# Optimization experiments

Hardware: AMD Instinct MI355X
Metric: run time of the kernel (lower is better)

The kernel has to match this reference:

```python
import jax, jax.numpy as jnp
import numpy as np

HID = 128  # hardcoded in the original module (hyperparameters['hidden_sizes'])
BETA1, BETA2, ADAM_EPS = 0.9, 0.999, 1e-8  # torch.optim.Adam defaults


def _xavier(k, shape):
    lim = np.sqrt(6.0 / (shape[0] + shape[1]))
    return jax.random.uniform(k, shape, jnp.float32, -lim, lim)


def setup_inputs() -> dict:
    key = jax.random.key(0)
    k0, k1, k2 = jax.random.split(key, 3)
    input_size, output_size = 65536, 4096
    return {
        "x": jax.random.uniform(k0, (input_size,), jnp.float32),
        "W1": _xavier(k1, (input_size, HID)),
        "W2": _xavier(k2, (HID, output_size)),
        "b_in": jnp.zeros((input_size,), jnp.float32),
        "b_h": jnp.zeros((HID,), jnp.float32),
        "b_out": jnp.zeros((output_size,), jnp.float32),
        "hidden0": jnp.zeros((HID,), jnp.float32),
        "output0": jnp.zeros((output_size,), jnp.float32),
        "n_iterations": 256,
        "epsilon": 0.01,
    }


def _drho(s):
    # gradient mask of rho = clamp(s, 0, 1), matching torch clamp backward
    return ((s >= 0.0) & (s <= 1.0)).astype(s.dtype)


def reference(x, W1, W2, b_in, b_h, b_out, hidden0, output0, n_iterations, epsilon):
    r_x = jnp.clip(x, 0.0, 1.0)
    xW1 = r_x @ W1  # [HID], constant across iterations (input is clamped/fixed)

    def adam(p, g, m, v, t1):
        m = BETA1 * m + (1.0 - BETA1) * g
        v = BETA2 * v + (1.0 - BETA2) * g * g
        mhat = m / (1.0 - jnp.power(BETA1, t1))
        vhat = v / (1.0 - jnp.power(BETA2, t1))
        return p - epsilon * mhat / (jnp.sqrt(vhat) + ADAM_EPS), m, v

    def step(carry, t):
        h, o, mh, vh, mo, vo = carry
        r_h = jnp.clip(h, 0.0, 1.0)
        r_o = jnp.clip(o, 0.0, 1.0)
        # analytic dE/dh, dE/do of the quadratic Hopfield energy
        g_h = _drho(h) * (r_h - b_h - xW1 - W2 @ r_o)      # [HID]
        g_o = _drho(o) * (r_o - b_out - r_h @ W2)          # [output_size]
        t1 = t + 1.0
        h, mh, vh = adam(h, g_h, mh, vh, t1)
        o, mo, vo = adam(o, g_o, mo, vo, t1)
        return (h, o, mh, vh, mo, vo), None

    init = (hidden0, output0,
            jnp.zeros_like(hidden0), jnp.zeros_like(hidden0),
            jnp.zeros_like(output0), jnp.zeros_like(output0))
    (h, o, *_), _ = jax.lax.scan(step, init, jnp.arange(n_iterations, dtype=jnp.float32))
    return o
```

## Files before the change

kernel.cpp:

```cpp
#include <hip/hip_runtime.h>
#include <stdint.h>

#define HID   128
#define OUT   4096
#define NWG   8
#define SLICE 512
#define NT    512
#define NXB   128
#define RPX   512

typedef unsigned long long u64;

__device__ __forceinline__ u64 pk(uint32_t tag, float v) {
  return ((u64)tag << 32) | (u64)__float_as_uint(v);
}

__global__ __launch_bounds__(NT, 1) void k_all(
    const float* __restrict__ x,
    const float* __restrict__ W1,
    const float* __restrict__ W2,
    const float* __restrict__ b_h,
    const float* __restrict__ b_out,
    const float* __restrict__ h0,
    const float* __restrict__ o0,
    const int* __restrict__ n_iter_p,
    const float* __restrict__ eps_p,
    u64* __restrict__ pbuf,
    u64* __restrict__ xw1p,
    float* __restrict__ out) {

  __shared__ __attribute__((aligned(16))) float red[8 * SLICE];
  __shared__ __attribute__((aligned(16))) float rh_s[HID];
  __shared__ __attribute__((aligned(16))) float ro_s[SLICE];

  const int t = threadIdx.x;

  if (blockIdx.x >= NWG) {
    const int b = blockIdx.x - NWG;
    const int c4 = (t & 31) * 4;
    const int rseg = t >> 5;
    const int r0 = b * RPX + rseg * 32;
    float4 acc = make_float4(0.f, 0.f, 0.f, 0.f);
#pragma unroll 8
    for (int k = 0; k < 32; ++k) {
      const int r = r0 + k;
      const float rx = fminf(fmaxf(x[r], 0.f), 1.f);
      const float4 wv = *(const float4*)&W1[(size_t)r * HID + c4];
      acc.x = fmaf(rx, wv.x, acc.x); acc.y = fmaf(rx, wv.y, acc.y);
      acc.z = fmaf(rx, wv.z, acc.z); acc.w = fmaf(rx, wv.w, acc.w);
    }
    *(float4*)&red[rseg * HID + c4] = acc;
    __syncthreads();
    if (t < HID) {
      float s = 0.f;
#pragma unroll
      for (int k = 0; k < 16; k += 4)
        s += (red[k*HID + t] + red[(k+1)*HID + t]) + (red[(k+2)*HID + t] + red[(k+3)*HID + t]);
      __hip_atomic_store(&xw1p[b * HID + t], pk(1u, s),
                         __ATOMIC_RELAXED, __HIP_MEMORY_SCOPE_AGENT);
    }
    return;
  }

  const int wg = blockIdx.x;
  const int cg = t & 63;
  const int rg = t >> 6;
  const int n_iter = *n_iter_p;
  const float eps  = *eps_p;

  float w2[16][8];
  {
    const float* wp = W2 + (size_t)(rg * 16) * OUT + wg * SLICE + cg;
#pragma unroll
    for (int r = 0; r < 16; ++r)
#pragma unroll
      for (int k = 0; k < 8; ++k)
        w2[r][k] = wp[(size_t)r * OUT + 64 * k];
  }
#pragma unroll
  for (int r = 0; r < 16; ++r)
    asm volatile("" : "+v"(w2[r][0]), "+v"(w2[r][1]), "+v"(w2[r][2]), "+v"(w2[r][3]),
                      "+v"(w2[r][4]), "+v"(w2[r][5]), "+v"(w2[r][6]), "+v"(w2[r][7]));

  float bhx = 0.f, hh = 0.f, mh = 0.f, vh = 0.f;
  if (t < HID) {
    float s = 0.f;
#pragma unroll 1
    for (int ch = 0; ch < 8; ++ch) {
      u64 v[16];
      for (;;) {
#pragma unroll
        for (int k = 0; k < 16; ++k)
          v[k] = __hip_atomic_load(&xw1p[(ch * 16 + k) * HID + t],
                                   __ATOMIC_RELAXED, __HIP_MEMORY_SCOPE_AGENT);
        uint32_t bad = 0u;
#pragma unroll
        for (int k = 0; k < 16; ++k) bad |= ((uint32_t)(v[k] >> 32)) ^ 1u;
        if (bad == 0u) break;
        __builtin_amdgcn_s_sleep(2);
      }
#pragma unroll
      for (int k = 0; k < 16; ++k) s += __uint_as_float((uint32_t)v[k]);
    }
    bhx = b_h[t] + s;
    hh  = h0[t];
    rh_s[t] = fminf(fmaxf(hh, 0.f), 1.f);
  }
  float oo = o0[wg * SLICE + t];
  float mo = 0.f, vo = 0.f;
  const float bo = b_out[wg * SLICE + t];
  ro_s[t] = fminf(fmaxf(oo, 0.f), 1.f);
  __syncthreads();

  float bp1 = 1.f, bp2 = 1.f;

  for (int it = 0; it < n_iter; ++it) {
    bp1 *= 0.9f; bp2 *= 0.999f;
    const float c1 = 1.f / (1.f - bp1);
    const float c2 = 1.f / (1.f - bp2);
    u64* pb = pbuf + (size_t)(it & 1) * (NWG * HID);
    const uint32_t tag = (uint32_t)(it + 1);

    float aB[16];
    {
      float rov[8];
#pragma unroll
      for (int k = 0; k < 8; ++k) rov[k] = ro_s[cg + 64 * k];
#pragma unroll
      for (int r = 0; r < 16; ++r) {
        float a = w2[r][0] * rov[0];
#pragma unroll
        for (int k = 1; k < 8; ++k) a = fmaf(w2[r][k], rov[k], a);
        aB[r] = a;
      }
    }
    {
#pragma unroll
      for (int r = 0; r < 8; ++r) {
        const float keep = (cg & 32) ? aB[r + 8] : aB[r];
        const float send = (cg & 32) ? aB[r]     : aB[r + 8];
        aB[r] = keep + __shfl_xor(send, 32, 64);
      }
#pragma unroll
      for (int r = 0; r < 4; ++r) {
        const float keep = (cg & 16) ? aB[r + 4] : aB[r];
        const float send = (cg & 16) ? aB[r]     : aB[r + 4];
        aB[r] = keep + __shfl_xor(send, 16, 64);
      }
#pragma unroll
      for (int r = 0; r < 2; ++r) {
        const float keep = (cg & 8) ? aB[r + 2] : aB[r];
        const float send = (cg & 8) ? aB[r]     : aB[r + 2];
        aB[r] = keep + __shfl_xor(send, 8, 64);
      }
      {
        const float keep = (cg & 4) ? aB[1] : aB[0];
        const float send = (cg & 4) ? aB[0] : aB[1];
        aB[0] = keep + __shfl_xor(send, 4, 64);
      }
      aB[0] += __shfl_xor(aB[0], 2, 64);
      aB[0] += __shfl_xor(aB[0], 1, 64);
    }
    if ((cg & 3) == 0) {
      __hip_atomic_store(&pb[wg * HID + rg * 16 + (cg >> 2)], pk(tag, aB[0]),
                         __ATOMIC_RELAXED, __HIP_MEMORY_SCOPE_AGENT);
    }

    {
      float aA[8] = {0.f, 0.f, 0.f, 0.f, 0.f, 0.f, 0.f, 0.f};
#pragma unroll
      for (int r = 0; r < 16; ++r) {
        const float rh = rh_s[rg * 16 + r];
#pragma unroll
        for (int k = 0; k < 8; ++k) aA[k] = fmaf(w2[r][k], rh, aA[k]);
      }
#pragma unroll
      for (int k = 0; k < 8; ++k)
        red[rg * SLICE + cg + 64 * k] = aA[k];
    }
    __syncthreads();

    {
      const float s = ((red[t] + red[SLICE + t]) + (red[2*SLICE + t] + red[3*SLICE + t]))
                    + ((red[4*SLICE + t] + red[5*SLICE + t]) + (red[6*SLICE + t] + red[7*SLICE + t]));
      const float ro_old = fminf(fmaxf(oo, 0.f), 1.f);
      const float g = (oo >= 0.f && oo <= 1.f) ? (ro_old - bo - s) : 0.f;
      mo = 0.9f * mo + 0.1f * g;
      vo = 0.999f * vo + 0.001f * g * g;
      oo -= eps * (mo * c1) / (sqrtf(vo * c2) + 1e-8f);
      ro_s[t] = fminf(fmaxf(oo, 0.f), 1.f);
    }

    if (t < HID) {
      float gv[8];
      for (;;) {
        u64 v[8];
#pragma unroll
        for (int wi = 0; wi < 8; ++wi)
          v[wi] = __hip_atomic_load(&pb[wi * HID + t],
                                    __ATOMIC_RELAXED, __HIP_MEMORY_SCOPE_AGENT);
        uint32_t bad = 0u;
#pragma unroll
        for (int wi = 0; wi < 8; ++wi) bad |= ((uint32_t)(v[wi] >> 32)) ^ tag;
        if (bad == 0u) {
#pragma unroll
          for (int wi = 0; wi < 8; ++wi) gv[wi] = __uint_as_float((uint32_t)v[wi]);
          break;
        }
        __builtin_amdgcn_s_sleep(1);
      }
      const float gsum = ((gv[0] + gv[1]) + (gv[2] + gv[3]))
                       + ((gv[4] + gv[5]) + (gv[6] + gv[7]));
      const float rh_old = fminf(fmaxf(hh, 0.f), 1.f);
      const float g = (hh >= 0.f && hh <= 1.f) ? (rh_old - bhx - gsum) : 0.f;
      mh = 0.9f * mh + 0.1f * g;
      vh = 0.999f * vh + 0.001f * g * g;
      hh -= eps * (mh * c1) / (sqrtf(vh * c2) + 1e-8f);
      rh_s[t] = fminf(fmaxf(hh, 0.f), 1.f);
    }
    __syncthreads();
  }

  out[wg * SLICE + t] = oo;
}

extern "C" void kernel_launch(void* const* d_in, const int* in_sizes, int n_in,
                              void* d_out, int out_size, void* d_ws, size_t ws_size,
                              hipStream_t stream) {
  const float* x     = (const float*)d_in[0];
  const float* W1    = (const float*)d_in[1];
  const float* W2    = (const float*)d_in[2];
  const float* b_h   = (const float*)d_in[4];
  const float* b_out = (const float*)d_in[5];
  const float* h0    = (const float*)d_in[6];
  const float* o0    = (const float*)d_in[7];
  const int*   nit   = (const int*)d_in[8];
  const float* eps   = (const float*)d_in[9];

  u64*   pbuf = (u64*)d_ws;
  u64*   xw1p = (u64*)((char*)d_ws + 16384);
  float* out  = (float*)d_out;

  k_all<<<dim3(NWG + NXB), dim3(NT), 0, stream>>>(x, W1, W2, b_h, b_out, h0, o0,
                                                  nit, eps, pbuf, xw1p, out);
}
```

Measured before the change: 605.2 us.

## Co-locate iterating workgroups on one XCD and use XCD-local flag polling

Each block reads its XCD id and takes a role dynamically, so all eight iterating workgroups land on the same XCD. The per-iteration partial-sum exchange can then publish to and poll through that XCD's shared L2 (sc0 stores and loads), avoiding device-scope coherence on every spin. A system-scope shadow copy is written and polled every eighth spin as a fallback, and the sleep in the spin loop is removed. This adds a memset launch, a startup election that all blocks wait on, and relies on the hardware-register XCD encoding and cache-policy bits being correct.

```diff
diff --git a/kernel.cpp b/kernel.cpp
--- a/kernel.cpp
+++ b/kernel.cpp
@@ -14,6 +14,7 @@
 __device__ __forceinline__ u64 pk(uint32_t tag, float v) {
   return ((u64)tag << 32) | (u64)__float_as_uint(v);
 }
+
 
 __global__ __launch_bounds__(NT, 1) void k_all(
     const float* __restrict__ x,
@@ -26,17 +27,43 @@
     const int* __restrict__ n_iter_p,
     const float* __restrict__ eps_p,
     u64* __restrict__ pbuf,
+    u64* __restrict__ pshad,
     u64* __restrict__ xw1p,
+    int* __restrict__ ctl,
     float* __restrict__ out) {
 
   __shared__ __attribute__((aligned(16))) float red[8 * SLICE];
   __shared__ __attribute__((aligned(16))) float rh_s[HID];
   __shared__ __attribute__((aligned(16))) float ro_s[SLICE];
+  __shared__ int s_role;
 
   const int t = threadIdx.x;
 
-  if (blockIdx.x >= NWG) {
-    const int b = blockIdx.x - NWG;
+  if (t == 0) {
+    const uint32_t xcd =
+        (uint32_t)__builtin_amdgcn_s_getreg((31 << 11) | 20) & 7u;
+    const int idx = __hip_atomic_fetch_add(&ctl[2 + (int)xcd], 1, __ATOMIC_RELAXED,
+                                           __HIP_MEMORY_SCOPE_AGENT);
+    if (idx == NWG - 1) {
+      int expected = 0;
+      __hip_atomic_compare_exchange_strong(&ctl[0], &expected, (int)xcd + 1,
+                                           __ATOMIC_RELAXED, __ATOMIC_RELAXED,
+                                           __HIP_MEMORY_SCOPE_AGENT);
+    }
+    int ch;
+    while ((ch = __hip_atomic_load(&ctl[0], __ATOMIC_RELAXED,
+                                   __HIP_MEMORY_SCOPE_AGENT)) == 0)
+      __builtin_amdgcn_s_sleep(8);
+    s_role = ((int)xcd + 1 == ch && idx < NWG)
+                 ? idx
+                 : NWG + __hip_atomic_fetch_add(&ctl[1], 1, __ATOMIC_RELAXED,
+                                                __HIP_MEMORY_SCOPE_AGENT);
+  }
+  __syncthreads();
+  const int role = s_role;
+
+  if (role >= NWG) {
+    const int b = role - NWG;
     const int c4 = (t & 31) * 4;
     const int rseg = t >> 5;
     const int r0 = b * RPX + rseg * 32;
@@ -62,7 +89,7 @@
     return;
   }
 
-  const int wg = blockIdx.x;
+  const int wg = role;
   const int cg = t & 63;
   const int rg = t >> 6;
   const int n_iter = *n_iter_p;
@@ -82,16 +109,24 @@
     asm volatile("" : "+v"(w2[r][0]), "+v"(w2[r][1]), "+v"(w2[r][2]), "+v"(w2[r][3]),
                       "+v"(w2[r][4]), "+v"(w2[r][5]), "+v"(w2[r][6]), "+v"(w2[r][7]));
 
+  const int prow = wg * HID + rg * 16 + (cg >> 2);
+  const u64 pubp0 = (u64)(uintptr_t)(pbuf + prow);
+  const u64 pubp1 = (u64)(uintptr_t)(pbuf + NWG * HID + prow);
+  const u64 pubs0 = (u64)(uintptr_t)(pshad + prow);
+  const u64 pubs1 = (u64)(uintptr_t)(pshad + NWG * HID + prow);
+  const u64 pol0  = (u64)(uintptr_t)(pbuf + t);
+  const u64 pol1  = (u64)(uintptr_t)(pbuf + NWG * HID + t);
+
   float bhx = 0.f, hh = 0.f, mh = 0.f, vh = 0.f;
   if (t < HID) {
     float s = 0.f;
 #pragma unroll 1
-    for (int ch = 0; ch < 8; ++ch) {
+    for (int chk = 0; chk < 8; ++chk) {
       u64 v[16];
       for (;;) {
 #pragma unroll
         for (int k = 0; k < 16; ++k)
-          v[k] = __hip_atomic_load(&xw1p[(ch * 16 + k) * HID + t],
+          v[k] = __hip_atomic_load(&xw1p[(chk * 16 + k) * HID + t],
                                    __ATOMIC_RELAXED, __HIP_MEMORY_SCOPE_AGENT);
         uint32_t bad = 0u;
 #pragma unroll
@@ -118,7 +153,6 @@
     bp1 *= 0.9f; bp2 *= 0.999f;
     const float c1 = 1.f / (1.f - bp1);
     const float c2 = 1.f / (1.f - bp2);
-    u64* pb = pbuf + (size_t)(it & 1) * (NWG * HID);
     const uint32_t tag = (uint32_t)(it + 1);
 
     float aB[16];
@@ -162,8 +196,11 @@
       aB[0] += __shfl_xor(aB[0], 1, 64);
     }
     if ((cg & 3) == 0) {
-      __hip_atomic_store(&pb[wg * HID + rg * 16 + (cg >> 2)], pk(tag, aB[0]),
-                         __ATOMIC_RELAXED, __HIP_MEMORY_SCOPE_AGENT);
+      const u64 val = pk(tag, aB[0]);
+      const u64 pp  = (it & 1) ? pubp1 : pubp0;
+      const u64 psd = (it & 1) ? pubs1 : pubs0;
+      asm volatile("global_store_dwordx2 %0, %1, off sc0" :: "v"(pp),  "v"(val) : "memory");
+      asm volatile("global_store_dwordx2 %0, %1, off sc0 sc1" :: "v"(psd), "v"(val) : "memory");
     }
 
     {
@@ -192,25 +229,52 @@
     }
 
     if (t < HID) {
-      float gv[8];
+      float g0, g1, g2, g3, g4, g5, g6, g7;
+      const u64 pa  = (it & 1) ? pol1 : pol0;
+      const u64 pb2 = pa + 4096;
+      const u64* ps = pshad + ((it & 1) ? NWG * HID : 0) + t;
+      int spin = 0;
       for (;;) {
-        u64 v[8];
-#pragma unroll
-        for (int wi = 0; wi < 8; ++wi)
-          v[wi] = __hip_atomic_load(&pb[wi * HID + t],
-                                    __ATOMIC_RELAXED, __HIP_MEMORY_SCOPE_AGENT);
-        uint32_t bad = 0u;
-#pragma unroll
-        for (int wi = 0; wi < 8; ++wi) bad |= ((uint32_t)(v[wi] >> 32)) ^ tag;
+        u64 v0, v1, v2, v3, v4, v5, v6, v7;
+        if (__builtin_expect((spin & 7) == 7, 0)) {
+          v0 = __hip_atomic_load(ps + 0*HID, __ATOMIC_RELAXED, __HIP_MEMORY_SCOPE_AGENT);
+          v1 = __hip_atomic_load(ps + 1*HID, __ATOMIC_RELAXED, __HIP_MEMORY_SCOPE_AGENT);
+          v2 = __hip_atomic_load(ps + 2*HID, __ATOMIC_RELAXED, __HIP_MEMORY_SCOPE_AGENT);
+          v3 = __hip_atomic_load(ps + 3*HID, __ATOMIC_RELAXED, __HIP_MEMORY_SCOPE_AGENT);
+          v4 = __hip_atomic_load(ps + 4*HID, __ATOMIC_RELAXED, __HIP_MEMORY_SCOPE_AGENT);
+          v5 = __hip_atomic_load(ps + 5*HID, __ATOMIC_RELAXED, __HIP_MEMORY_SCOPE_AGENT);
+          v6 = __hip_atomic_load(ps + 6*HID, __ATOMIC_RELAXED, __HIP_MEMORY_SCOPE_AGENT);
+          v7 = __hip_atomic_load(ps + 7*HID, __ATOMIC_RELAXED, __HIP_MEMORY_SCOPE_AGENT);
+        } else {
+          asm volatile(
+              "global_load_dwordx2 %0, %8, off sc0\n\t"
+              "global_load_dwordx2 %1, %8, off offset:1024 sc0\n\t"
+              "global_load_dwordx2 %2, %8, off offset:2048 sc0\n\t"
+              "global_load_dwordx2 %3, %8, off offset:3072 sc0\n\t"
+              "global_load_dwordx2 %4, %9, off sc0\n\t"
+              "global_load_dwordx2 %5, %9, off offset:1024 sc0\n\t"
+              "global_load_dwordx2 %6, %9, off offset:2048 sc0\n\t"
+              "global_load_dwordx2 %7, %9, off offset:3072 sc0\n\t"
+              "s_waitcnt vmcnt(0)"
+              : "=&v"(v0), "=&v"(v1), "=&v"(v2), "=&v"(v3),
+                "=&v"(v4), "=&v"(v5), "=&v"(v6), "=&v"(v7)
+              : "v"(pa), "v"(pb2)
+              : "memory");
+        }
+        const uint32_t bad = (((uint32_t)(v0 >> 32)) ^ tag) | (((uint32_t)(v1 >> 32)) ^ tag)
+                           | (((uint32_t)(v2 >> 32)) ^ tag) | (((uint32_t)(v3 >> 32)) ^ tag)
+                           | (((uint32_t)(v4 >> 32)) ^ tag) | (((uint32_t)(v5 >> 32)) ^ tag)
+                           | (((uint32_t)(v6 >> 32)) ^ tag) | (((uint32_t)(v7 >> 32)) ^ tag);
         if (bad == 0u) {
-#pragma unroll
-          for (int wi = 0; wi < 8; ++wi) gv[wi] = __uint_as_float((uint32_t)v[wi]);
+          g0 = __uint_as_float((uint32_t)v0); g1 = __uint_as_float((uint32_t)v1);
+          g2 = __uint_as_float((uint32_t)v2); g3 = __uint_as_float((uint32_t)v3);
+          g4 = __uint_as_float((uint32_t)v4); g5 = __uint_as_float((uint32_t)v5);
+          g6 = __uint_as_float((uint32_t)v6); g7 = __uint_as_float((uint32_t)v7);
           break;
         }
-        __builtin_amdgcn_s_sleep(1);
-      }
-      const float gsum = ((gv[0] + gv[1]) + (gv[2] + gv[3]))
-                       + ((gv[4] + gv[5]) + (gv[6] + gv[7]));
+        ++spin;
+      }
+      const float gsum = ((g0 + g1) + (g2 + g3)) + ((g4 + g5) + (g6 + g7));
       const float rh_old = fminf(fmaxf(hh, 0.f), 1.f);
       const float g = (hh >= 0.f && hh <= 1.f) ? (rh_old - bhx - gsum) : 0.f;
       mh = 0.9f * mh + 0.1f * g;
@@ -237,10 +301,13 @@
   const int*   nit   = (const int*)d_in[8];
   const float* eps   = (const float*)d_in[9];
 
-  u64*   pbuf = (u64*)d_ws;
-  u64*   xw1p = (u64*)((char*)d_ws + 16384);
-  float* out  = (float*)d_out;
-
+  u64* pbuf  = (u64*)d_ws;
+  u64* pshad = (u64*)((char*)d_ws + 16384);
+  u64* xw1p  = (u64*)((char*)d_ws + 32768);
+  int* ctl   = (int*)((char*)d_ws + 163840);
+  float* out = (float*)d_out;
+
+  hipMemsetAsync(ctl, 0, 64, stream);
   k_all<<<dim3(NWG + NXB), dim3(NT), 0, stream>>>(x, W1, W2, b_h, b_out, h0, o0,
-                                                  nit, eps, pbuf, xw1p, out);
+                                                  nit, eps, pbuf, pshad, xw1p, ctl, out);
 }
```

New measurement: 1.059 ms. 1.75x slower.

## Defer hidden-state update one iteration to overlap cross-workgroup exchange with compute

Applied to the files above, without the earlier changes.

The hidden-state Adam update for step it-1 now runs inside step it, after the W2·r_o partial products are computed. Each step still publishes its partials before the r_h·W2 product, and the update reads them from the previous step's slot, first trying a speculative prefetch issued at the end of that step. This lets the global-memory handoff between workgroups overlap local compute instead of stalling right after the output update. The partial buffer grows to four rotating slots so a slot is not overwritten while slower workgroups may still read it, and the workspace offset moves to match. Barriers are replaced by explicit lgkmcnt-wait plus s_barrier wrappers, with three barriers per step instead of two.

```diff
diff --git a/kernel.cpp b/kernel.cpp
--- a/kernel.cpp
+++ b/kernel.cpp
@@ -8,11 +8,19 @@
 #define NT    512
 #define NXB   128
 #define RPX   512
+#define NSLOT 4
 
 typedef unsigned long long u64;
 
 __device__ __forceinline__ u64 pk(uint32_t tag, float v) {
   return ((u64)tag << 32) | (u64)__float_as_uint(v);
+}
+
+__device__ __forceinline__ void bar_lgkm() {
+  __builtin_amdgcn_sched_barrier(0);
+  asm volatile("s_waitcnt lgkmcnt(0)" ::: "memory");
+  __builtin_amdgcn_s_barrier();
+  __builtin_amdgcn_sched_barrier(0);
 }
 
 __global__ __launch_bounds__(NT, 1) void k_all(
@@ -113,14 +121,9 @@
   __syncthreads();
 
   float bp1 = 1.f, bp2 = 1.f;
+  u64 pref[8] = {0, 0, 0, 0, 0, 0, 0, 0};
 
   for (int it = 0; it < n_iter; ++it) {
-    bp1 *= 0.9f; bp2 *= 0.999f;
-    const float c1 = 1.f / (1.f - bp1);
-    const float c2 = 1.f / (1.f - bp2);
-    u64* pb = pbuf + (size_t)(it & 1) * (NWG * HID);
-    const uint32_t tag = (uint32_t)(it + 1);
-
     float aB[16];
     {
       float rov[8];
@@ -161,10 +164,54 @@
       aB[0] += __shfl_xor(aB[0], 2, 64);
       aB[0] += __shfl_xor(aB[0], 1, 64);
     }
+
+    if (t < HID && it > 0) {
+      const uint32_t tagc = (uint32_t)it;
+      u64 v[8];
+#pragma unroll
+      for (int wi = 0; wi < 8; ++wi) v[wi] = pref[wi];
+      uint32_t bad = 0u;
+#pragma unroll
+      for (int wi = 0; wi < 8; ++wi) bad |= ((uint32_t)(v[wi] >> 32)) ^ tagc;
+      if (bad != 0u) {
+        u64* pc = pbuf + (size_t)((it - 1) & (NSLOT - 1)) * (NWG * HID);
+        do {
+#pragma unroll
+          for (int wi = 0; wi < 8; ++wi)
+            v[wi] = __hip_atomic_load(&pc[wi * HID + t],
+                                      __ATOMIC_RELAXED, __HIP_MEMORY_SCOPE_AGENT);
+          bad = 0u;
+#pragma unroll
+          for (int wi = 0; wi < 8; ++wi) bad |= ((uint32_t)(v[wi] >> 32)) ^ tagc;
+          if (bad != 0u) __builtin_amdgcn_s_sleep(1);
+        } while (bad != 0u);
+      }
+      const float gsum = ((__uint_as_float((uint32_t)v[0]) + __uint_as_float((uint32_t)v[1]))
+                        + (__uint_as_float((uint32_t)v[2]) + __uint_as_float((uint32_t)v[3])))
+                       + ((__uint_as_float((uint32_t)v[4]) + __uint_as_float((uint32_t)v[5]))
+                        + (__uint_as_float((uint32_t)v[6]) + __uint_as_float((uint32_t)v[7])));
+      const float c1h = 1.f / (1.f - bp1);
+      const float c2h = 1.f / (1.f - bp2);
+      const float rh_old = fminf(fmaxf(hh, 0.f), 1.f);
+      const float g = (hh >= 0.f && hh <= 1.f) ? (rh_old - bhx - gsum) : 0.f;
+      mh = 0.9f * mh + 0.1f * g;
+      vh = 0.999f * vh + 0.001f * g * g;
+      hh -= eps * (mh * c1h) / (sqrtf(vh * c2h) + 1e-8f);
+      rh_s[t] = fminf(fmaxf(hh, 0.f), 1.f);
+    }
+
     if ((cg & 3) == 0) {
-      __hip_atomic_store(&pb[wg * HID + rg * 16 + (cg >> 2)], pk(tag, aB[0]),
+      u64* pp = pbuf + (size_t)(it & (NSLOT - 1)) * (NWG * HID)
+                     + wg * HID + rg * 16 + (cg >> 2);
+      __hip_atomic_store(pp, pk((uint32_t)(it + 1), aB[0]),
                          __ATOMIC_RELAXED, __HIP_MEMORY_SCOPE_AGENT);
     }
+
+    bp1 *= 0.9f; bp2 *= 0.999f;
+    const float c1 = 1.f / (1.f - bp1);
+    const float c2 = 1.f / (1.f - bp2);
+
+    bar_lgkm();
 
     {
       float aA[8] = {0.f, 0.f, 0.f, 0.f, 0.f, 0.f, 0.f, 0.f};
@@ -178,7 +225,7 @@
       for (int k = 0; k < 8; ++k)
         red[rg * SLICE + cg + 64 * k] = aA[k];
     }
-    __syncthreads();
+    bar_lgkm();
 
     {
       const float s = ((red[t] + red[SLICE + t]) + (red[2*SLICE + t] + red[3*SLICE + t]))
@@ -191,34 +238,15 @@
       ro_s[t] = fminf(fmaxf(oo, 0.f), 1.f);
     }
 
-    if (t < HID) {
-      float gv[8];
-      for (;;) {
-        u64 v[8];
-#pragma unroll
-        for (int wi = 0; wi < 8; ++wi)
-          v[wi] = __hip_atomic_load(&pb[wi * HID + t],
-                                    __ATOMIC_RELAXED, __HIP_MEMORY_SCOPE_AGENT);
-        uint32_t bad = 0u;
-#pragma unroll
-        for (int wi = 0; wi < 8; ++wi) bad |= ((uint32_t)(v[wi] >> 32)) ^ tag;
-        if (bad == 0u) {
-#pragma unroll
-          for (int wi = 0; wi < 8; ++wi) gv[wi] = __uint_as_float((uint32_t)v[wi]);
-          break;
-        }
-        __builtin_amdgcn_s_sleep(1);
-      }
-      const float gsum = ((gv[0] + gv[1]) + (gv[2] + gv[3]))
-                       + ((gv[4] + gv[5]) + (gv[6] + gv[7]));
-      const float rh_old = fminf(fmaxf(hh, 0.f), 1.f);
-      const float g = (hh >= 0.f && hh <= 1.f) ? (rh_old - bhx - gsum) : 0.f;
-      mh = 0.9f * mh + 0.1f * g;
-      vh = 0.999f * vh + 0.001f * g * g;
-      hh -= eps * (mh * c1) / (sqrtf(vh * c2) + 1e-8f);
-      rh_s[t] = fminf(fmaxf(hh, 0.f), 1.f);
-    }
-    __syncthreads();
+    if (t < HID && it + 1 < n_iter) {
+      const u64* pn = pbuf + (size_t)(it & (NSLOT - 1)) * (NWG * HID);
+#pragma unroll
+      for (int wi = 0; wi < 8; ++wi)
+        pref[wi] = __hip_atomic_load(&pn[wi * HID + t],
+                                     __ATOMIC_RELAXED, __HIP_MEMORY_SCOPE_AGENT);
+    }
+
+    bar_lgkm();
   }
 
   out[wg * SLICE + t] = oo;
@@ -238,7 +266,7 @@
   const float* eps   = (const float*)d_in[9];
 
   u64*   pbuf = (u64*)d_ws;
-  u64*   xw1p = (u64*)((char*)d_ws + 16384);
+  u64*   xw1p = (u64*)((char*)d_ws + 32768);
   float* out  = (float*)d_out;
 
   k_all<<<dim3(NWG + NXB), dim3(NT), 0, stream>>>(x, W1, W2, b_h, b_out, h0, o0,
```

Result: faster. 551.6 us (-8.9%).
